# Optimization experiments

Hardware: AMD Instinct MI355X
Metric: run time of the kernel (lower is better)

The kernel has to match this reference:

```python
import jax, jax.numpy as jnp
import numpy as np

N = 100000   # nodes
E = 1600000  # edges
F = 128      # in = hidden channels
L = 4        # num GCN layers
G = 512      # graphs in batch
OUT = 10     # classes
EPS = 1e-5


def setup_inputs() -> dict:
    key = jax.random.key(0)
    ks = jax.random.split(key, 12)
    x = jax.random.normal(ks[0], (N, F), dtype=jnp.float32)
    edge_index = jax.random.randint(ks[1], (2, E), 0, N, dtype=jnp.int64)
    batch = jnp.sort(jax.random.randint(ks[2], (N,), 0, G, dtype=jnp.int64))
    s = 1.0 / np.sqrt(F)
    Ws = jax.random.uniform(ks[3], (L, F, F), jnp.float32, -s, s)
    bs = jax.random.uniform(ks[4], (L, F), jnp.float32, -s, s)
    gammas = jnp.ones((L, F), jnp.float32)
    betas = jnp.zeros((L, F), jnp.float32)
    s1 = 1.0 / np.sqrt(F * L)
    W1 = jax.random.uniform(ks[5], (F * L, F), jnp.float32, -s1, s1)
    b1 = jax.random.uniform(ks[6], (F,), jnp.float32, -s1, s1)
    g1 = jnp.ones((F,), jnp.float32)
    bt1 = jnp.zeros((F,), jnp.float32)
    s2 = 1.0 / np.sqrt(F)
    W2 = jax.random.uniform(ks[7], (F, OUT), jnp.float32, -s2, s2)
    b2 = jax.random.uniform(ks[8], (OUT,), jnp.float32, -s2, s2)
    return {"x": x, "edge_index": edge_index, "batch": batch, "Ws": Ws, "bs": bs,
            "gammas": gammas, "betas": betas, "W1": W1, "b1": b1, "g1": g1,
            "bt1": bt1, "W2": W2, "b2": b2}


def _batch_norm(x, g, b):
    # training-mode BatchNorm1d over the node dim (biased variance)
    mu = jnp.mean(x, axis=0)
    var = jnp.var(x, axis=0)
    return (x - mu) * jax.lax.rsqrt(var + EPS) * g + b


def reference(x, edge_index, batch, Ws, bs, gammas, betas, W1, b1, g1, bt1, W2, b2):
    row, col = edge_index[0], edge_index[1]
    # GCN normalization (add_self_loops=False since normalize=True)
    deg = jax.ops.segment_sum(jnp.ones((E,), x.dtype), col, num_segments=N)
    dinv = jnp.where(deg > 0, jax.lax.rsqrt(deg), 0.0)
    norm = dinv[row] * dinv[col]  # [E]
    pooled = []
    h = x
    for t in range(L):
        hw = h @ Ws[t]                                    # [N, F]
        msg = norm[:, None] * hw[row]                     # gather  [E, F]
        h = jax.ops.segment_sum(msg, col, num_segments=N) + bs[t]  # scatter [N, F]
        h = jax.nn.relu(h)
        h = _batch_norm(h, gammas[t], betas[t])
        pooled.append(jax.ops.segment_sum(h, batch, num_segments=G))  # [G, F]
    z = jnp.concatenate(pooled, axis=1)                   # [G, L*F]
    z = z @ W1 + b1
    z = _batch_norm(z, g1, bt1)
    z = jax.nn.relu(z)
    return z @ W2 + b2                                    # [G, OUT]
```

## Files before the change

### kernel.cpp

```cpp
#include <hip/hip_runtime.h>

#define NN 100000
#define EE 1600000
#define FF 128
#define LL 4
#define GG 512
#define OUTC 10
#define EPSF 1e-5f
#define NSCB ((NN + 255) / 256)

typedef __attribute__((ext_vector_type(8))) short short8;
typedef __attribute__((ext_vector_type(4))) float f32x4;

__device__ inline unsigned bf16rne(float f) {
  unsigned u = __float_as_uint(f);
  return (u + 0x7fffu + ((u >> 16) & 1u)) >> 16;
}
__device__ inline unsigned packbf(float lo, float hi) {
  return bf16rne(lo) | (bf16rne(hi) << 16);
}
__device__ inline float bflo(unsigned u) { return __uint_as_float(u << 16); }
__device__ inline float bfhi(unsigned u) { return __uint_as_float(u & 0xffff0000u); }


__global__ __launch_bounds__(256) void k_deg(const int* __restrict__ col, int* __restrict__ deg) {
  int e = blockIdx.x * 256 + threadIdx.x;
  if (e < EE) atomicAdd(&deg[col[e]], 1);
}

__global__ __launch_bounds__(256) void k_dinv(const int* __restrict__ deg, float* __restrict__ dinv) {
  int n = blockIdx.x * 256 + threadIdx.x;
  if (n < NN) {
    int d = deg[n];
    dinv[n] = d > 0 ? rsqrtf((float)d) : 0.0f;
  }
}

__global__ __launch_bounds__(256) void k_bsum(const int* __restrict__ deg, int* __restrict__ bsum) {
  int i = blockIdx.x * 256 + threadIdx.x;
  int v = (i < NN) ? deg[i] : 0;
#pragma unroll
  for (int off = 32; off > 0; off >>= 1) v += __shfl_down(v, off, 64);
  __shared__ int ws[4];
  if ((threadIdx.x & 63) == 0) ws[threadIdx.x >> 6] = v;
  __syncthreads();
  if (threadIdx.x == 0) bsum[blockIdx.x] = ws[0] + ws[1] + ws[2] + ws[3];
}

__global__ __launch_bounds__(256) void k_rowptr(const int* __restrict__ deg,
                                                const int* __restrict__ bsum,
                                                int* __restrict__ rowptr) {
  __shared__ int sb[512];
  __shared__ int sd[256];
  const int t = threadIdx.x;
  sb[t]       = (t < NSCB) ? bsum[t] : 0;
  sb[t + 256] = (t + 256 < NSCB) ? bsum[t + 256] : 0;
  __syncthreads();
#pragma unroll
  for (int off = 1; off < 512; off <<= 1) {
    int v0 = (t >= off) ? sb[t - off] : 0;
    int v1 = sb[t + 256 - off];
    __syncthreads();
    sb[t] += v0;
    sb[t + 256] += v1;
    __syncthreads();
  }
  const int bpre = (blockIdx.x == 0) ? 0 : sb[blockIdx.x - 1];
  const int i = blockIdx.x * 256 + t;
  const int d = (i < NN) ? deg[i] : 0;
  sd[t] = d;
  __syncthreads();
#pragma unroll
  for (int off = 1; off < 256; off <<= 1) {
    int v = (t >= off) ? sd[t - off] : 0;
    __syncthreads();
    sd[t] += v;
    __syncthreads();
  }
  if (i < NN) rowptr[i] = bpre + sd[t] - d;
  if (blockIdx.x == 0 && t == 0) rowptr[NN] = EE;
}

__global__ __launch_bounds__(256) void k_fill(const int* __restrict__ ei,
                                              const int* __restrict__ rowptr,
                                              int* __restrict__ cnt,
                                              const float* __restrict__ dinv,
                                              int2* __restrict__ ecw) {
  int e = blockIdx.x * 256 + threadIdx.x;
  if (e >= EE) return;
  int r = ei[e];
  int cl = ei[EE + e];
  int slot = rowptr[cl] + atomicAdd(&cnt[cl], 1);
  ecw[slot] = make_int2(r, __float_as_int(dinv[r] * dinv[cl]));
}

__global__ __launch_bounds__(256) void k_bounds(const int* __restrict__ batch, int* __restrict__ gstart) {
  int n = blockIdx.x * 256 + threadIdx.x;
  if (n >= NN) return;
  int b = batch[n];
  if (n == 0) {
    for (int g = 0; g <= b; ++g) gstart[g] = 0;
  } else {
    int bp = batch[n - 1];
    for (int g = bp + 1; g <= b; ++g) gstart[g] = n;
  }
  if (n == NN - 1) {
    for (int g = b + 1; g <= GG; ++g) gstart[g] = NN;
  }
}


__global__ __launch_bounds__(256) void k_cvt(const float* __restrict__ x, unsigned* __restrict__ Ab) {
  int i = blockIdx.x * 256 + threadIdx.x;
  if (i < NN * 64) {
    float2 v = *(const float2*)(x + (size_t)i * 2);
    Ab[i] = packbf(v.x, v.y);
  }
}

__global__ __launch_bounds__(256) void k_wcvt(const float* __restrict__ Ws, uint4* __restrict__ Wf) {
  int tid = blockIdx.x * 256 + threadIdx.x;
  int t = tid >> 12;
  int r = tid & 4095;
  int lane = r & 63;
  int which = (r >> 6) & 1;
  int ct = (r >> 7) & 7;
  int kc = r >> 10;
  int n = ct * 16 + (lane & 15);
  int k0 = kc * 32 + (lane >> 4) * 8;
  const float* W = Ws + t * 16384;
  unsigned h[8];
#pragma unroll
  for (int j = 0; j < 8; ++j) {
    float w = W[(k0 + j) * 128 + n];
    unsigned hb = bf16rne(w);
    if (which == 0) {
      h[j] = hb;
    } else {
      float hf = __uint_as_float(hb << 16);
      h[j] = bf16rne(w - hf);
    }
  }
  uint4 o;
  o.x = h[0] | (h[1] << 16);
  o.y = h[2] | (h[3] << 16);
  o.z = h[4] | (h[5] << 16);
  o.w = h[6] | (h[7] << 16);
  Wf[tid] = o;
}

__global__ __launch_bounds__(256) void k_mm(const unsigned* __restrict__ Ab,
                                            const uint4* __restrict__ Wf,
                                            unsigned* __restrict__ Bb) {
  const int lane = threadIdx.x & 63;
  const int w = threadIdx.x >> 6;
  const int quad = lane >> 4;
  const int m = lane & 15;
  const int rowbase = blockIdx.x * 64 + w * 16;
  const int arow = min(rowbase + m, NN - 1);
  const uint4* A4 = (const uint4*)Ab;
  f32x4 acc[8];
#pragma unroll
  for (int ct = 0; ct < 8; ++ct) acc[ct] = (f32x4){0.f, 0.f, 0.f, 0.f};
#pragma unroll
  for (int kc = 0; kc < 4; ++kc) {
    uint4 av = A4[arow * 16 + kc * 4 + quad];
    short8 af = *(short8*)&av;
#pragma unroll
    for (int ct = 0; ct < 8; ++ct) {
      uint4 bh = Wf[((kc * 8 + ct) * 2 + 0) * 64 + lane];
      uint4 bl = Wf[((kc * 8 + ct) * 2 + 1) * 64 + lane];
      acc[ct] = __builtin_amdgcn_mfma_f32_16x16x32_bf16(af, *(short8*)&bh, acc[ct], 0, 0, 0);
      acc[ct] = __builtin_amdgcn_mfma_f32_16x16x32_bf16(af, *(short8*)&bl, acc[ct], 0, 0, 0);
    }
  }
#pragma unroll
  for (int ct = 0; ct < 8; ++ct) {
#pragma unroll
    for (int r = 0; r < 4; ++r) {
      float v = acc[ct][r];
      float vo = __shfl_xor(v, 1);
      int row = rowbase + quad * 4 + r;
      if ((lane & 1) == 0 && row < NN) {
        Bb[row * 64 + ct * 8 + (m >> 1)] = packbf(v, vo);
      }
    }
  }
}

__global__ __launch_bounds__(256) void k_agg(const unsigned* __restrict__ Bb,
                                             const int* __restrict__ rowptr,
                                             const int2* __restrict__ ecw,
                                             const float* __restrict__ bias,
                                             unsigned* __restrict__ Ar,
                                             float* __restrict__ bnbuf) {
  const int lane = threadIdx.x & 63;
  const int wave = threadIdx.x >> 6;
  const int c = lane * 2;
  const int gwave = blockIdx.x * 4 + wave;
  const int nwaves = gridDim.x * 4;
  const float2 bv = *(const float2*)(bias + c);
  float s0 = 0.f, s1 = 0.f, q0 = 0.f, q1 = 0.f;
  for (int n = gwave; n < NN; n += nwaves) {
    const int beg = rowptr[n];
    const int end = rowptr[n + 1];
    float ax[8], ay[8];
#pragma unroll
    for (int j = 0; j < 8; ++j) { ax[j] = 0.f; ay[j] = 0.f; }
    int2 stage = (beg + lane < end) ? ecw[beg + lane] : make_int2(0, 0);
    for (int base = beg; base < end; base += 64) {
      const int2 cur = stage;
      const int nb = base + 64;
      if (nb < end) {
        const int j = nb + lane;
        stage = (j < end) ? ecw[j] : make_int2(0, 0);
      }
#pragma unroll
      for (int g = 0; g < 4; ++g) {
        if (base + g * 16 < end) {
          int is[16]; float wv[16]; unsigned us[16];
#pragma unroll
          for (int j = 0; j < 16; ++j) {
            is[j] = __shfl(cur.x, g * 16 + j);
            wv[j] = __shfl(__int_as_float(cur.y), g * 16 + j);
          }
#pragma unroll
          for (int j = 0; j < 16; ++j) us[j] = Bb[((unsigned)is[j] << 6) + (unsigned)lane];
#pragma unroll
          for (int j = 0; j < 16; ++j) {
            ax[j & 7] = fmaf(wv[j], bflo(us[j]), ax[j & 7]);
            ay[j & 7] = fmaf(wv[j], bfhi(us[j]), ay[j & 7]);
          }
        }
      }
    }
    float rx = ((ax[0] + ax[1]) + (ax[2] + ax[3])) + ((ax[4] + ax[5]) + (ax[6] + ax[7]));
    float ry = ((ay[0] + ay[1]) + (ay[2] + ay[3])) + ((ay[4] + ay[5]) + (ay[6] + ay[7]));
    rx = fmaxf(rx + bv.x, 0.f);
    ry = fmaxf(ry + bv.y, 0.f);
    Ar[(size_t)n * 64 + lane] = packbf(rx, ry);
    s0 += rx; s1 += ry;
    q0 = fmaf(rx, rx, q0); q1 = fmaf(ry, ry, q1);
  }
  __shared__ float sred[4][256];
  sred[wave][c] = s0;
  sred[wave][c + 1] = s1;
  sred[wave][128 + c] = q0;
  sred[wave][128 + c + 1] = q1;
  __syncthreads();
  const int t = threadIdx.x;
  float tot = sred[0][t] + sred[1][t] + sred[2][t] + sred[3][t];
  atomicAdd(&bnbuf[t], tot);
}

__global__ __launch_bounds__(128) void k_bnfin(const float* __restrict__ bnbuf,
                                               const float* __restrict__ gamma,
                                               const float* __restrict__ beta,
                                               float* __restrict__ bnsc) {
  const int c = threadIdx.x;
  float mu = bnbuf[c] * (1.0f / NN);
  float var = bnbuf[128 + c] * (1.0f / NN) - mu * mu;
  float inv = rsqrtf(var + EPSF);
  float sc = gamma[c] * inv;
  bnsc[c] = sc;
  bnsc[128 + c] = beta[c] - mu * sc;
}

__global__ __launch_bounds__(128) void k_bnapply(const unsigned* __restrict__ Ar,
                                                 const float* __restrict__ bnsc,
                                                 const int* __restrict__ gstart,
                                                 float* __restrict__ pooledt,
                                                 unsigned* __restrict__ Ab) {
  const int g = blockIdx.x >> 3;
  const int sub = blockIdx.x & 7;
  const int s = gstart[g];
  const int e = gstart[g + 1];
  const int cnt = e - s;
  if (cnt <= 0) return;
  const int per = (cnt + 7) >> 3;
  const int ns = s + sub * per;
  const int ne = min(ns + per, e);
  if (ns >= ne) return;
  const int cp = threadIdx.x & 63;
  const int half = threadIdx.x >> 6;
  const float2 sc = *(const float2*)(bnsc + 2 * cp);
  const float2 sh = *(const float2*)(bnsc + 128 + 2 * cp);
  float accx = 0.f, accy = 0.f;
  for (int n = ns + half; n < ne; n += 2) {
    unsigned u = Ar[(size_t)n * 64 + cp];
    float vx = fmaf(bflo(u), sc.x, sh.x);
    float vy = fmaf(bfhi(u), sc.y, sh.y);
    Ab[(size_t)n * 64 + cp] = packbf(vx, vy);
    accx += vx;
    accy += vy;
  }
  atomicAdd(&pooledt[(size_t)g * 512 + 2 * cp], accx);
  atomicAdd(&pooledt[(size_t)g * 512 + 2 * cp + 1], accy);
}


__global__ __launch_bounds__(128) void k_z1(const float* __restrict__ pooled,
                                            const float* __restrict__ W1,
                                            const float* __restrict__ b1,
                                            float* __restrict__ z1) {
  __shared__ float sp[512];
  const int g = blockIdx.x;
  for (int i = threadIdx.x; i < 512; i += 128) sp[i] = pooled[(size_t)g * 512 + i];
  __syncthreads();
  const int c = threadIdx.x;
  float acc = b1[c];
  for (int j = 0; j < 512; ++j) acc = fmaf(sp[j], W1[j * 128 + c], acc);
  z1[(size_t)g * 128 + c] = acc;
}

__global__ __launch_bounds__(128) void k_zstat(const float* __restrict__ z1,
                                               const float* __restrict__ g1,
                                               const float* __restrict__ bt1,
                                               float* __restrict__ zsc) {
  const int c = threadIdx.x;
  float s = 0.f, q = 0.f;
  for (int g = 0; g < GG; ++g) {
    float v = z1[g * 128 + c];
    s += v;
    q = fmaf(v, v, q);
  }
  float mu = s * (1.0f / GG);
  float var = q * (1.0f / GG) - mu * mu;
  float inv = rsqrtf(var + EPSF);
  float sc = g1[c] * inv;
  zsc[c] = sc;
  zsc[128 + c] = bt1[c] - mu * sc;
}

__global__ __launch_bounds__(128) void k_out(const float* __restrict__ z1,
                                             const float* __restrict__ zsc,
                                             const float* __restrict__ W2,
                                             const float* __restrict__ b2,
                                             float* __restrict__ out) {
  __shared__ float zr[128];
  const int g = blockIdx.x;
  const int c = threadIdx.x;
  zr[c] = fmaxf(fmaf(z1[(size_t)g * 128 + c], zsc[c], zsc[128 + c]), 0.f);
  __syncthreads();
  if (c < OUTC) {
    float acc = b2[c];
    for (int k = 0; k < 128; ++k) acc = fmaf(zr[k], W2[k * OUTC + c], acc);
    out[(size_t)g * OUTC + c] = acc;
  }
}


extern "C" void kernel_launch(void* const* d_in, const int* in_sizes, int n_in,
                              void* d_out, int out_size, void* d_ws, size_t ws_size,
                              hipStream_t stream) {
  const float* x      = (const float*)d_in[0];
  const int*   ei     = (const int*)d_in[1];
  const int*   batch  = (const int*)d_in[2];
  const float* Ws     = (const float*)d_in[3];
  const float* bs     = (const float*)d_in[4];
  const float* gammas = (const float*)d_in[5];
  const float* betas  = (const float*)d_in[6];
  const float* W1     = (const float*)d_in[7];
  const float* b1     = (const float*)d_in[8];
  const float* g1     = (const float*)d_in[9];
  const float* bt1    = (const float*)d_in[10];
  const float* W2     = (const float*)d_in[11];
  const float* b2     = (const float*)d_in[12];
  float* out = (float*)d_out;

  char* ws = (char*)d_ws;
  size_t off = 0;
  auto alloc = [&](size_t bytes) -> void* {
    void* p = ws + off;
    off = (off + bytes + 255) & ~(size_t)255;
    return p;
  };
  int*   deg    = (int*)alloc((size_t)NN * 4);
  int*   cnt    = (int*)alloc((size_t)NN * 4);
  float* bnbuf  = (float*)alloc((size_t)LL * 256 * 4);
  float* pooled = (float*)alloc((size_t)GG * 512 * 4);
  size_t zero_bytes = off;
  unsigned* Ar     = (unsigned*)alloc((size_t)NN * 64 * 4);
  unsigned* Ab     = (unsigned*)alloc((size_t)NN * 64 * 4);
  unsigned* Bb     = (unsigned*)alloc((size_t)NN * 64 * 4);
  int2*     ecw    = (int2*)alloc((size_t)EE * 8);
  float*    dinv   = (float*)alloc((size_t)NN * 4);
  int*      rowptr = (int*)alloc((size_t)(NN + 1) * 4);
  int*      bsum   = (int*)alloc((size_t)NSCB * 4);
  int*      gstart = (int*)alloc((size_t)(GG + 1) * 4);
  uint4*    Wf     = (uint4*)alloc((size_t)LL * 4096 * 16);
  float*    z1     = (float*)alloc((size_t)GG * FF * 4);
  float*    bnsc   = (float*)alloc(256 * 4);
  float*    zsc    = (float*)alloc(256 * 4);
  (void)ws_size; (void)in_sizes; (void)n_in; (void)out_size;

  hipMemsetAsync(d_ws, 0, zero_bytes, stream);

  k_deg<<<(EE + 255) / 256, 256, 0, stream>>>(ei + EE, deg);
  k_dinv<<<(NN + 255) / 256, 256, 0, stream>>>(deg, dinv);
  k_bsum<<<NSCB, 256, 0, stream>>>(deg, bsum);
  k_rowptr<<<NSCB, 256, 0, stream>>>(deg, bsum, rowptr);
  k_fill<<<(EE + 255) / 256, 256, 0, stream>>>(ei, rowptr, cnt, dinv, ecw);
  k_bounds<<<(NN + 255) / 256, 256, 0, stream>>>(batch, gstart);
  k_cvt<<<(NN * 64 + 255) / 256, 256, 0, stream>>>(x, Ab);
  k_wcvt<<<64, 256, 0, stream>>>(Ws, Wf);

  for (int t = 0; t < LL; ++t) {
    k_mm<<<(NN + 63) / 64, 256, 0, stream>>>(Ab, Wf + (size_t)t * 4096, Bb);
    k_agg<<<2048, 256, 0, stream>>>(Bb, rowptr, ecw, bs + t * FF, Ar, bnbuf + t * 256);
    k_bnfin<<<1, 128, 0, stream>>>(bnbuf + t * 256, gammas + t * FF, betas + t * FF, bnsc);
    k_bnapply<<<GG * 8, 128, 0, stream>>>(Ar, bnsc, gstart, pooled + t * FF, Ab);
  }

  k_z1<<<GG, 128, 0, stream>>>(pooled, W1, b1, z1);
  k_zstat<<<1, 128, 0, stream>>>(z1, g1, bt1, zsc);
  k_out<<<GG, 128, 0, stream>>>(z1, zsc, W2, b2, out);
}
```

Before: 854.9 us.

## Aggregate a contiguous run of 16 nodes per wave with a shared edge stream

Each wave now owns 16 consecutive destination nodes and walks their combined CSR edge range as one stream in 64-edge chunks, closing out a node whenever the running edge index reaches its row end. Edge indices and weights are staged through LDS and broadcast with readfirstlane instead of per-edge shuffles. This is meant to stop low-degree nodes (about 16 edges on average) from leaving most of each 64-edge chunk idle, and to cut shuffle overhead. In exchange it adds per-edge boundary checks and a serial dependency on two accumulators instead of eight, which can lengthen FMA chains.

```diff
diff --git a/kernel.cpp b/kernel.cpp
--- a/kernel.cpp
+++ b/kernel.cpp
@@ -8,6 +8,10 @@
 #define OUTC 10
 #define EPSF 1e-5f
 #define NSCB ((NN + 255) / 256)
+
+#define NPW 16
+#define AGG_WAVES ((NN + NPW - 1) / NPW)
+#define AGG_BLOCKS ((AGG_WAVES + 3) / 4)
 
 typedef __attribute__((ext_vector_type(8))) short short8;
 typedef __attribute__((ext_vector_type(4))) float f32x4;
@@ -198,49 +202,74 @@
   const int wave = threadIdx.x >> 6;
   const int c = lane * 2;
   const int gwave = blockIdx.x * 4 + wave;
-  const int nwaves = gridDim.x * 4;
+  const int n0 = gwave * NPW;
   const float2 bv = *(const float2*)(bias + c);
   float s0 = 0.f, s1 = 0.f, q0 = 0.f, q1 = 0.f;
-  for (int n = gwave; n < NN; n += nwaves) {
-    const int beg = rowptr[n];
-    const int end = rowptr[n + 1];
-    float ax[8], ay[8];
-#pragma unroll
-    for (int j = 0; j < 8; ++j) { ax[j] = 0.f; ay[j] = 0.f; }
-    int2 stage = (beg + lane < end) ? ecw[beg + lane] : make_int2(0, 0);
-    for (int base = beg; base < end; base += 64) {
-      const int2 cur = stage;
+  __shared__ int srp[4][NPW + 1];
+  __shared__ int2 sstage[4][64];
+  if (n0 < NN) {
+    const int nn = min(NPW, NN - n0);
+    if (lane <= nn) srp[wave][lane] = rowptr[n0 + lane];
+    float ax0 = 0.f, ax1 = 0.f, ay0 = 0.f, ay1 = 0.f;
+    auto finalize = [&](int node) {
+      float rx = fmaxf(ax0 + ax1 + bv.x, 0.f);
+      float ry = fmaxf(ay0 + ay1 + bv.y, 0.f);
+      Ar[(size_t)(n0 + node) * 64 + lane] = packbf(rx, ry);
+      s0 += rx; s1 += ry;
+      q0 = fmaf(rx, rx, q0); q1 = fmaf(ry, ry, q1);
+      ax0 = 0.f; ax1 = 0.f; ay0 = 0.f; ay1 = 0.f;
+    };
+    const int beg = __builtin_amdgcn_readfirstlane(srp[wave][0]);
+    const int endall = __builtin_amdgcn_readfirstlane(srp[wave][nn]);
+    int cn = 0;
+    while (cn < nn && __builtin_amdgcn_readfirstlane(srp[wave][cn + 1]) == beg) {
+      finalize(cn);
+      ++cn;
+    }
+    int nend = (cn < nn) ? __builtin_amdgcn_readfirstlane(srp[wave][cn + 1]) : 0x7fffffff;
+    int2 stage = (beg + lane < endall) ? ecw[beg + lane] : make_int2(0, 0);
+    for (int base = beg; base < endall; base += 64) {
+      sstage[wave][lane] = stage;
       const int nb = base + 64;
-      if (nb < end) {
-        const int j = nb + lane;
-        stage = (j < end) ? ecw[j] : make_int2(0, 0);
+      if (nb < endall) {
+        stage = (nb + lane < endall) ? ecw[nb + lane] : make_int2(0, 0);
       }
 #pragma unroll
       for (int g = 0; g < 4; ++g) {
-        if (base + g * 16 < end) {
-          int is[16]; float wv[16]; unsigned us[16];
+        if (base + g * 16 < endall) {
+          int2 ew[16]; unsigned us[16];
+#pragma unroll
+          for (int j = 0; j < 16; ++j) ew[j] = sstage[wave][g * 16 + j];
 #pragma unroll
           for (int j = 0; j < 16; ++j) {
-            is[j] = __shfl(cur.x, g * 16 + j);
-            wv[j] = __shfl(__int_as_float(cur.y), g * 16 + j);
+            const int sj = __builtin_amdgcn_readfirstlane(ew[j].x);
+            us[j] = Bb[((size_t)(unsigned)sj << 6) + (unsigned)lane];
           }
 #pragma unroll
-          for (int j = 0; j < 16; ++j) us[j] = Bb[((unsigned)is[j] << 6) + (unsigned)lane];
-#pragma unroll
           for (int j = 0; j < 16; ++j) {
-            ax[j & 7] = fmaf(wv[j], bflo(us[j]), ax[j & 7]);
-            ay[j & 7] = fmaf(wv[j], bfhi(us[j]), ay[j & 7]);
+            const float wj = __int_as_float(ew[j].y);
+            if (j & 1) {
+              ax1 = fmaf(wj, bflo(us[j]), ax1);
+              ay1 = fmaf(wj, bfhi(us[j]), ay1);
+            } else {
+              ax0 = fmaf(wj, bflo(us[j]), ax0);
+              ay0 = fmaf(wj, bfhi(us[j]), ay0);
+            }
+            const int e1 = base + g * 16 + j + 1;
+            if (e1 == nend) {
+              finalize(cn);
+              ++cn;
+              nend = (cn < nn) ? __builtin_amdgcn_readfirstlane(srp[wave][cn + 1]) : 0x7fffffff;
+              while (cn < nn && nend == e1) {
+                finalize(cn);
+                ++cn;
+                nend = (cn < nn) ? __builtin_amdgcn_readfirstlane(srp[wave][cn + 1]) : 0x7fffffff;
+              }
+            }
           }
         }
       }
     }
-    float rx = ((ax[0] + ax[1]) + (ax[2] + ax[3])) + ((ax[4] + ax[5]) + (ax[6] + ax[7]));
-    float ry = ((ay[0] + ay[1]) + (ay[2] + ay[3])) + ((ay[4] + ay[5]) + (ay[6] + ay[7]));
-    rx = fmaxf(rx + bv.x, 0.f);
-    ry = fmaxf(ry + bv.y, 0.f);
-    Ar[(size_t)n * 64 + lane] = packbf(rx, ry);
-    s0 += rx; s1 += ry;
-    q0 = fmaf(rx, rx, q0); q1 = fmaf(ry, ry, q1);
   }
   __shared__ float sred[4][256];
   sred[wave][c] = s0;
@@ -407,7 +436,7 @@
 
   for (int t = 0; t < LL; ++t) {
     k_mm<<<(NN + 63) / 64, 256, 0, stream>>>(Ab, Wf + (size_t)t * 4096, Bb);
-    k_agg<<<2048, 256, 0, stream>>>(Bb, rowptr, ecw, bs + t * FF, Ar, bnbuf + t * 256);
+    k_agg<<<AGG_BLOCKS, 256, 0, stream>>>(Bb, rowptr, ecw, bs + t * FF, Ar, bnbuf + t * 256);
     k_bnfin<<<1, 128, 0, stream>>>(bnbuf + t * 256, gammas + t * FF, betas + t * FF, bnsc);
     k_bnapply<<<GG * 8, 128, 0, stream>>>(Ar, bnsc, gstart, pooled + t * FF, Ab);
   }
```

Result: no change. 840.4 us (-1.7%).
